# Kernel optimization log

Measured on AMD Instinct MI355X. Metric: run time of the kernel, lower is better.

The kernel has to match this reference:

```python
import jax, jax.numpy as jnp
import numpy as np

A_MIN = 0.001
EPS = 1e-08


def setup_inputs() -> dict:
    key = jax.random.key(0)
    k1, k2, k3, k4 = jax.random.split(key, 4)
    B, O, I = 512, 1024, 512
    x = jax.random.normal(k1, (B, I), dtype=jnp.float32)
    translation = jax.random.uniform(k2, (O, I), dtype=jnp.float32, minval=-1.0, maxval=1.0)
    scale_raw = jax.random.uniform(k3, (O, I), dtype=jnp.float32, minval=-2.0, maxval=0.0)
    weights = jax.random.normal(k4, (O, I), dtype=jnp.float32) * (1.0 / np.sqrt(I))
    return {"x": x, "translation": translation, "scale_raw": scale_raw, "weights": weights}


def reference(x, translation, scale_raw, weights):
    # x: (B, I); params: (O, I)
    scale = A_MIN + jax.nn.softplus(scale_raw)  # (O, I)
    # s: (B, O, I) broadcast intermediate
    s = (x[:, None, :] - translation[None, :, :]) / (scale[None, :, :] + EPS)
    s2 = s * s
    wavelet = (1.0 - s2) * jnp.exp(-0.5 * s2)  # mexican hat
    y = jnp.einsum('oi,boi->bo', weights, wavelet)  # reduce over in_features
    return y
```

## Files before the change

### kernel.cpp

```cpp
#include <hip/hip_runtime.h>


#define WL_A_MIN 0.001f
#define WL_EPS   1e-8f

constexpr int WL_B = 512;
constexpr int WL_O = 1024;
constexpr int WL_I = 512;

#define WL_SQK  0.84932180553704583800f
#define WL_IK   1.38629436111989061883f
#define WL_L2E  1.44269504088896340736f
#define WL_LN2  0.69314718055994530942f

typedef float v2f __attribute__((ext_vector_type(2)));

struct P3 { float nti, inv, w; };

__device__ __forceinline__ float fast_exp2(float a) {
#if __has_builtin(__builtin_amdgcn_exp2f)
    return __builtin_amdgcn_exp2f(a);
#else
    return exp2f(a);
#endif
}
__device__ __forceinline__ float fast_log2(float a) {
#if __has_builtin(__builtin_amdgcn_logf)
    return __builtin_amdgcn_logf(a);
#else
    return __log2f(a);
#endif
}
__device__ __forceinline__ float fast_rcp(float a) {
#if __has_builtin(__builtin_amdgcn_rcpf)
    return __builtin_amdgcn_rcpf(a);
#else
    return 1.0f / a;
#endif
}

__global__ __launch_bounds__(256) void wl_prep(
    const float* __restrict__ translation,
    const float* __restrict__ scale_raw,
    const float* __restrict__ weights,
    P3* __restrict__ pT3)
{
    __shared__ P3 lds[16 * 64];
    const int t  = threadIdx.x;
    const int o0 = blockIdx.x * 64;
    const int i0 = blockIdx.y * 16;

    {
        const int o_l = t >> 2;
        const int iq  = t & 3;
        const size_t g = (size_t)(o0 + o_l) * WL_I + (i0 + iq * 4);
        const float4 tv = *reinterpret_cast<const float4*>(translation + g);
        const float4 sv = *reinterpret_cast<const float4*>(scale_raw   + g);
        const float4 wv = *reinterpret_cast<const float4*>(weights     + g);
        const float tt[4] = {tv.x, tv.y, tv.z, tv.w};
        const float ss[4] = {sv.x, sv.y, sv.z, sv.w};
        const float ww[4] = {wv.x, wv.y, wv.z, wv.w};
        #pragma unroll
        for (int j = 0; j < 4; ++j) {
            float ex  = fast_exp2(ss[j] * WL_L2E);
            float sp  = fast_log2(1.0f + ex) * WL_LN2;
            float inv = fast_rcp(WL_A_MIN + sp + WL_EPS) * WL_SQK;
            P3 pv; pv.nti = -tt[j] * inv; pv.inv = inv; pv.w = ww[j];
            lds[(iq * 4 + j) * 64 + o_l] = pv;
        }
    }
    __syncthreads();
    {
        const int o_l = t & 63;
        const int r   = t >> 6;
        #pragma unroll
        for (int j = 0; j < 4; ++j) {
            const int i_l = r * 4 + j;
            pT3[(size_t)(i0 + i_l) * WL_O + (o0 + o_l)] = lds[i_l * 64 + o_l];
        }
    }
}

__global__ __launch_bounds__(512, 8) void wl_main(
    const float* __restrict__ x,
    const P3* __restrict__ pT3,
    float* __restrict__ out)
{
    __shared__ float smem[5120];

    const int tid  = threadIdx.x;
    const int lane = tid & 63;
    const int wid  = tid >> 6;
    const int o    = blockIdx.x * 64 + lane;
    const int b0   = blockIdx.y * 8;

    {
        const int b_l = tid & 7;
        const int seg = tid >> 3;
        const float* xg = &x[(size_t)(b0 + b_l) * WL_I + seg * 8];
        const float4 v0 = *reinterpret_cast<const float4*>(xg);
        const float4 v1 = *reinterpret_cast<const float4*>(xg + 4);
        const int base = seg * 64 + b_l;
        smem[base +  0] = v0.x;
        smem[base +  8] = v0.y;
        smem[base + 16] = v0.z;
        smem[base + 24] = v0.w;
        smem[base + 32] = v1.x;
        smem[base + 40] = v1.y;
        smem[base + 48] = v1.z;
        smem[base + 56] = v1.w;
    }
    __syncthreads();

    const P3*    pp = pT3 + (size_t)(wid * 64) * WL_O + o;
    const float* xr = &smem[wid * 64 * 8];

    v2f aE0 = {0.f,0.f}, aE1 = {0.f,0.f}, aE2 = {0.f,0.f}, aE3 = {0.f,0.f};
    v2f aU0 = {0.f,0.f}, aU1 = {0.f,0.f}, aU2 = {0.f,0.f}, aU3 = {0.f,0.f};

    #pragma unroll 4
    for (int ii = 0; ii < 64; ++ii) {
        const P3 p = *pp;  pp += WL_O;
        const float4 xa = *reinterpret_cast<const float4*>(xr);
        const float4 xb = *reinterpret_cast<const float4*>(xr + 4);
        xr += 8;

        v2f nti = {p.nti, p.nti};
        v2f inv = {p.inv, p.inv};
        v2f wv  = {p.w,  p.w};

        v2f x01 = {xa.x, xa.y};
        v2f x23 = {xa.z, xa.w};
        v2f x45 = {xb.x, xb.y};
        v2f x67 = {xb.z, xb.w};

        v2f s0 = __builtin_elementwise_fma(x01, inv, nti);
        v2f s1 = __builtin_elementwise_fma(x23, inv, nti);
        v2f s2 = __builtin_elementwise_fma(x45, inv, nti);
        v2f s3 = __builtin_elementwise_fma(x67, inv, nti);
        v2f u0 = s0 * s0;
        v2f u1 = s1 * s1;
        v2f u2 = s2 * s2;
        v2f u3 = s3 * s3;
        v2f e0 = {fast_exp2(-u0.x), fast_exp2(-u0.y)};
        v2f e1 = {fast_exp2(-u1.x), fast_exp2(-u1.y)};
        v2f e2 = {fast_exp2(-u2.x), fast_exp2(-u2.y)};
        v2f e3 = {fast_exp2(-u3.x), fast_exp2(-u3.y)};
        aE0 = __builtin_elementwise_fma(wv, e0, aE0);
        aE1 = __builtin_elementwise_fma(wv, e1, aE1);
        aE2 = __builtin_elementwise_fma(wv, e2, aE2);
        aE3 = __builtin_elementwise_fma(wv, e3, aE3);
        v2f ue0 = u0 * e0;
        v2f ue1 = u1 * e1;
        v2f ue2 = u2 * e2;
        v2f ue3 = u3 * e3;
        aU0 = __builtin_elementwise_fma(wv, ue0, aU0);
        aU1 = __builtin_elementwise_fma(wv, ue1, aU1);
        aU2 = __builtin_elementwise_fma(wv, ue2, aU2);
        aU3 = __builtin_elementwise_fma(wv, ue3, aU3);
    }

    __syncthreads();
    constexpr int RS = 20;
    if (wid >= 4) {
        float4* dst = reinterpret_cast<float4*>(&smem[((wid - 4) * 64 + lane) * RS]);
        dst[0] = make_float4(aE0.x, aE0.y, aE1.x, aE1.y);
        dst[1] = make_float4(aE2.x, aE2.y, aE3.x, aE3.y);
        dst[2] = make_float4(aU0.x, aU0.y, aU1.x, aU1.y);
        dst[3] = make_float4(aU2.x, aU2.y, aU3.x, aU3.y);
    }
    __syncthreads();
    if (wid < 4) {
        const float4* src = reinterpret_cast<const float4*>(&smem[(wid * 64 + lane) * RS]);
        const float4 v0 = src[0], v1 = src[1], v2 = src[2], v3 = src[3];
        aE0.x += v0.x; aE0.y += v0.y; aE1.x += v0.z; aE1.y += v0.w;
        aE2.x += v1.x; aE2.y += v1.y; aE3.x += v1.z; aE3.y += v1.w;
        aU0.x += v2.x; aU0.y += v2.y; aU1.x += v2.z; aU1.y += v2.w;
        aU2.x += v3.x; aU2.y += v3.y; aU3.x += v3.z; aU3.y += v3.w;
    }
    __syncthreads();
    if (wid >= 1 && wid < 4) {
        float4* dst = reinterpret_cast<float4*>(&smem[((wid - 1) * 64 + lane) * RS]);
        dst[0] = make_float4(aE0.x, aE0.y, aE1.x, aE1.y);
        dst[1] = make_float4(aE2.x, aE2.y, aE3.x, aE3.y);
        dst[2] = make_float4(aU0.x, aU0.y, aU1.x, aU1.y);
        dst[3] = make_float4(aU2.x, aU2.y, aU3.x, aU3.y);
    }
    __syncthreads();
    if (wid == 0) {
        float E[8] = {aE0.x, aE0.y, aE1.x, aE1.y, aE2.x, aE2.y, aE3.x, aE3.y};
        float U[8] = {aU0.x, aU0.y, aU1.x, aU1.y, aU2.x, aU2.y, aU3.x, aU3.y};
        #pragma unroll
        for (int q = 0; q < 3; ++q) {
            const float4* src = reinterpret_cast<const float4*>(&smem[(q * 64 + lane) * RS]);
            const float4 v0 = src[0], v1 = src[1], v2 = src[2], v3 = src[3];
            E[0] += v0.x; E[1] += v0.y; E[2] += v0.z; E[3] += v0.w;
            E[4] += v1.x; E[5] += v1.y; E[6] += v1.z; E[7] += v1.w;
            U[0] += v2.x; U[1] += v2.y; U[2] += v2.z; U[3] += v2.w;
            U[4] += v3.x; U[5] += v3.y; U[6] += v3.z; U[7] += v3.w;
        }
        #pragma unroll
        for (int k = 0; k < 8; ++k)
            out[(size_t)(b0 + k) * WL_O + o] = fmaf(-WL_IK, U[k], E[k]);
    }
}

extern "C" void kernel_launch(void* const* d_in, const int* in_sizes, int n_in,
                              void* d_out, int out_size, void* d_ws, size_t ws_size,
                              hipStream_t stream) {
    const float* x           = (const float*)d_in[0];
    const float* translation = (const float*)d_in[1];
    const float* scale_raw   = (const float*)d_in[2];
    const float* weights     = (const float*)d_in[3];
    float*       out         = (float*)d_out;
    P3*          pT3         = (P3*)d_ws;

    wl_prep<<<dim3(WL_O / 64, WL_I / 16), dim3(256), 0, stream>>>(
        translation, scale_raw, weights, pT3);

    wl_main<<<dim3(WL_O / 64, WL_B / 8), dim3(512), 0, stream>>>(
        x, pT3, out);
}
```

Baseline: 109.7 us.

## Split parameter layout into paired v2f arrays and use op_sel packed FMAs

The transposed parameter buffer changes from a 12-byte struct into an 8-byte (nti,inv) array plus a weight array that packs two input indices per element. Loads are aligned 8-byte vectors, and inline-asm v_pk_fma_f32 with op_sel broadcasts scalars inside the packed op. This is meant to remove the per-iteration v_mov broadcast instructions. The cross-wave reduction becomes a single padded LDS transpose with two barriers instead of a multi-stage tree. Launch bounds drop the waves-per-EU hint from 8 to 6, and shared memory grows, which may reduce occupancy.

```diff
diff --git a/kernel.cpp b/kernel.cpp
--- a/kernel.cpp
+++ b/kernel.cpp
@@ -39,11 +39,56 @@
 #endif
 }
 
+#define WL_STEP(PA, PW, OS, XA, XB)                                            \
+  do {                                                                         \
+    v2f x01 = {(XA).x, (XA).y}, x23 = {(XA).z, (XA).w};                        \
+    v2f x45 = {(XB).x, (XB).y}, x67 = {(XB).z, (XB).w};                        \
+    v2f s0_, s1_, s2_, s3_, u0_, u1_, u2_, u3_;                                \
+    v2f e0_, e1_, e2_, e3_, t0_, t1_, t2_, t3_;                                \
+    asm("v_pk_fma_f32 %0, %1, %2, %2 op_sel:[0,1,0] op_sel_hi:[1,1,0]"         \
+        : "=v"(s0_) : "v"(x01), "v"(PA));                                      \
+    asm("v_pk_fma_f32 %0, %1, %2, %2 op_sel:[0,1,0] op_sel_hi:[1,1,0]"         \
+        : "=v"(s1_) : "v"(x23), "v"(PA));                                      \
+    asm("v_pk_fma_f32 %0, %1, %2, %2 op_sel:[0,1,0] op_sel_hi:[1,1,0]"         \
+        : "=v"(s2_) : "v"(x45), "v"(PA));                                      \
+    asm("v_pk_fma_f32 %0, %1, %2, %2 op_sel:[0,1,0] op_sel_hi:[1,1,0]"         \
+        : "=v"(s3_) : "v"(x67), "v"(PA));                                      \
+    asm("v_pk_mul_f32 %0, %1, %1" : "=v"(u0_) : "v"(s0_));                     \
+    asm("v_pk_mul_f32 %0, %1, %1" : "=v"(u1_) : "v"(s1_));                     \
+    asm("v_pk_mul_f32 %0, %1, %1" : "=v"(u2_) : "v"(s2_));                     \
+    asm("v_pk_mul_f32 %0, %1, %1" : "=v"(u3_) : "v"(s3_));                     \
+    e0_.x = fast_exp2(-u0_.x); e0_.y = fast_exp2(-u0_.y);                      \
+    e1_.x = fast_exp2(-u1_.x); e1_.y = fast_exp2(-u1_.y);                      \
+    e2_.x = fast_exp2(-u2_.x); e2_.y = fast_exp2(-u2_.y);                      \
+    e3_.x = fast_exp2(-u3_.x); e3_.y = fast_exp2(-u3_.y);                      \
+    asm("v_pk_fma_f32 %0, %1, %2, %0 op_sel:[" OS ",0,0] op_sel_hi:[" OS ",1,1]" \
+        : "+v"(aE0) : "v"(PW), "v"(e0_));                                      \
+    asm("v_pk_fma_f32 %0, %1, %2, %0 op_sel:[" OS ",0,0] op_sel_hi:[" OS ",1,1]" \
+        : "+v"(aE1) : "v"(PW), "v"(e1_));                                      \
+    asm("v_pk_fma_f32 %0, %1, %2, %0 op_sel:[" OS ",0,0] op_sel_hi:[" OS ",1,1]" \
+        : "+v"(aE2) : "v"(PW), "v"(e2_));                                      \
+    asm("v_pk_fma_f32 %0, %1, %2, %0 op_sel:[" OS ",0,0] op_sel_hi:[" OS ",1,1]" \
+        : "+v"(aE3) : "v"(PW), "v"(e3_));                                      \
+    asm("v_pk_mul_f32 %0, %1, %2" : "=v"(t0_) : "v"(u0_), "v"(e0_));           \
+    asm("v_pk_mul_f32 %0, %1, %2" : "=v"(t1_) : "v"(u1_), "v"(e1_));           \
+    asm("v_pk_mul_f32 %0, %1, %2" : "=v"(t2_) : "v"(u2_), "v"(e2_));           \
+    asm("v_pk_mul_f32 %0, %1, %2" : "=v"(t3_) : "v"(u3_), "v"(e3_));           \
+    asm("v_pk_fma_f32 %0, %1, %2, %0 op_sel:[" OS ",0,0] op_sel_hi:[" OS ",1,1]" \
+        : "+v"(aU0) : "v"(PW), "v"(t0_));                                      \
+    asm("v_pk_fma_f32 %0, %1, %2, %0 op_sel:[" OS ",0,0] op_sel_hi:[" OS ",1,1]" \
+        : "+v"(aU1) : "v"(PW), "v"(t1_));                                      \
+    asm("v_pk_fma_f32 %0, %1, %2, %0 op_sel:[" OS ",0,0] op_sel_hi:[" OS ",1,1]" \
+        : "+v"(aU2) : "v"(PW), "v"(t2_));                                      \
+    asm("v_pk_fma_f32 %0, %1, %2, %0 op_sel:[" OS ",0,0] op_sel_hi:[" OS ",1,1]" \
+        : "+v"(aU3) : "v"(PW), "v"(t3_));                                      \
+  } while (0)
+
 __global__ __launch_bounds__(256) void wl_prep(
     const float* __restrict__ translation,
     const float* __restrict__ scale_raw,
     const float* __restrict__ weights,
-    P3* __restrict__ pT3)
+    v2f* __restrict__ A2,
+    v2f* __restrict__ W2)
 {
     __shared__ P3 lds[16 * 64];
     const int t  = threadIdx.x;
@@ -73,20 +118,26 @@
     {
         const int o_l = t & 63;
         const int r   = t >> 6;
-        #pragma unroll
-        for (int j = 0; j < 4; ++j) {
-            const int i_l = r * 4 + j;
-            pT3[(size_t)(i0 + i_l) * WL_O + (o0 + o_l)] = lds[i_l * 64 + o_l];
+        const int o   = o0 + o_l;
+        #pragma unroll
+        for (int jp = 0; jp < 2; ++jp) {
+            const int i_l = r * 4 + jp * 2;
+            P3 a = lds[i_l * 64 + o_l];
+            P3 b = lds[(i_l + 1) * 64 + o_l];
+            A2[(size_t)(i0 + i_l)     * WL_O + o] = (v2f){a.nti, a.inv};
+            A2[(size_t)(i0 + i_l + 1) * WL_O + o] = (v2f){b.nti, b.inv};
+            W2[(size_t)((i0 + i_l) >> 1) * WL_O + o] = (v2f){a.w, b.w};
         }
     }
 }
 
-__global__ __launch_bounds__(512, 8) void wl_main(
+__global__ __launch_bounds__(512, 6) void wl_main(
     const float* __restrict__ x,
-    const P3* __restrict__ pT3,
+    const v2f* __restrict__ A2,
+    const v2f* __restrict__ W2,
     float* __restrict__ out)
 {
-    __shared__ float smem[5120];
+    __shared__ float smem[16 * 513];
 
     const int tid  = threadIdx.x;
     const int lane = tid & 63;
@@ -112,96 +163,46 @@
     }
     __syncthreads();
 
-    const P3*    pp = pT3 + (size_t)(wid * 64) * WL_O + o;
+    const v2f* __restrict__ pA = A2 + (size_t)(wid * 64) * WL_O + o;
+    const v2f* __restrict__ pW = W2 + (size_t)(wid * 32) * WL_O + o;
     const float* xr = &smem[wid * 64 * 8];
 
     v2f aE0 = {0.f,0.f}, aE1 = {0.f,0.f}, aE2 = {0.f,0.f}, aE3 = {0.f,0.f};
     v2f aU0 = {0.f,0.f}, aU1 = {0.f,0.f}, aU2 = {0.f,0.f}, aU3 = {0.f,0.f};
 
-    #pragma unroll 4
-    for (int ii = 0; ii < 64; ++ii) {
-        const P3 p = *pp;  pp += WL_O;
-        const float4 xa = *reinterpret_cast<const float4*>(xr);
-        const float4 xb = *reinterpret_cast<const float4*>(xr + 4);
-        xr += 8;
-
-        v2f nti = {p.nti, p.nti};
-        v2f inv = {p.inv, p.inv};
-        v2f wv  = {p.w,  p.w};
-
-        v2f x01 = {xa.x, xa.y};
-        v2f x23 = {xa.z, xa.w};
-        v2f x45 = {xb.x, xb.y};
-        v2f x67 = {xb.z, xb.w};
-
-        v2f s0 = __builtin_elementwise_fma(x01, inv, nti);
-        v2f s1 = __builtin_elementwise_fma(x23, inv, nti);
-        v2f s2 = __builtin_elementwise_fma(x45, inv, nti);
-        v2f s3 = __builtin_elementwise_fma(x67, inv, nti);
-        v2f u0 = s0 * s0;
-        v2f u1 = s1 * s1;
-        v2f u2 = s2 * s2;
-        v2f u3 = s3 * s3;
-        v2f e0 = {fast_exp2(-u0.x), fast_exp2(-u0.y)};
-        v2f e1 = {fast_exp2(-u1.x), fast_exp2(-u1.y)};
-        v2f e2 = {fast_exp2(-u2.x), fast_exp2(-u2.y)};
-        v2f e3 = {fast_exp2(-u3.x), fast_exp2(-u3.y)};
-        aE0 = __builtin_elementwise_fma(wv, e0, aE0);
-        aE1 = __builtin_elementwise_fma(wv, e1, aE1);
-        aE2 = __builtin_elementwise_fma(wv, e2, aE2);
-        aE3 = __builtin_elementwise_fma(wv, e3, aE3);
-        v2f ue0 = u0 * e0;
-        v2f ue1 = u1 * e1;
-        v2f ue2 = u2 * e2;
-        v2f ue3 = u3 * e3;
-        aU0 = __builtin_elementwise_fma(wv, ue0, aU0);
-        aU1 = __builtin_elementwise_fma(wv, ue1, aU1);
-        aU2 = __builtin_elementwise_fma(wv, ue2, aU2);
-        aU3 = __builtin_elementwise_fma(wv, ue3, aU3);
-    }
-
-    __syncthreads();
-    constexpr int RS = 20;
-    if (wid >= 4) {
-        float4* dst = reinterpret_cast<float4*>(&smem[((wid - 4) * 64 + lane) * RS]);
-        dst[0] = make_float4(aE0.x, aE0.y, aE1.x, aE1.y);
-        dst[1] = make_float4(aE2.x, aE2.y, aE3.x, aE3.y);
-        dst[2] = make_float4(aU0.x, aU0.y, aU1.x, aU1.y);
-        dst[3] = make_float4(aU2.x, aU2.y, aU3.x, aU3.y);
-    }
-    __syncthreads();
-    if (wid < 4) {
-        const float4* src = reinterpret_cast<const float4*>(&smem[(wid * 64 + lane) * RS]);
-        const float4 v0 = src[0], v1 = src[1], v2 = src[2], v3 = src[3];
-        aE0.x += v0.x; aE0.y += v0.y; aE1.x += v0.z; aE1.y += v0.w;
-        aE2.x += v1.x; aE2.y += v1.y; aE3.x += v1.z; aE3.y += v1.w;
-        aU0.x += v2.x; aU0.y += v2.y; aU1.x += v2.z; aU1.y += v2.w;
-        aU2.x += v3.x; aU2.y += v3.y; aU3.x += v3.z; aU3.y += v3.w;
-    }
-    __syncthreads();
-    if (wid >= 1 && wid < 4) {
-        float4* dst = reinterpret_cast<float4*>(&smem[((wid - 1) * 64 + lane) * RS]);
-        dst[0] = make_float4(aE0.x, aE0.y, aE1.x, aE1.y);
-        dst[1] = make_float4(aE2.x, aE2.y, aE3.x, aE3.y);
-        dst[2] = make_float4(aU0.x, aU0.y, aU1.x, aU1.y);
-        dst[3] = make_float4(aU2.x, aU2.y, aU3.x, aU3.y);
-    }
-    __syncthreads();
-    if (wid == 0) {
-        float E[8] = {aE0.x, aE0.y, aE1.x, aE1.y, aE2.x, aE2.y, aE3.x, aE3.y};
-        float U[8] = {aU0.x, aU0.y, aU1.x, aU1.y, aU2.x, aU2.y, aU3.x, aU3.y};
-        #pragma unroll
-        for (int q = 0; q < 3; ++q) {
-            const float4* src = reinterpret_cast<const float4*>(&smem[(q * 64 + lane) * RS]);
-            const float4 v0 = src[0], v1 = src[1], v2 = src[2], v3 = src[3];
-            E[0] += v0.x; E[1] += v0.y; E[2] += v0.z; E[3] += v0.w;
-            E[4] += v1.x; E[5] += v1.y; E[6] += v1.z; E[7] += v1.w;
-            U[0] += v2.x; U[1] += v2.y; U[2] += v2.z; U[3] += v2.w;
-            U[4] += v3.x; U[5] += v3.y; U[6] += v3.z; U[7] += v3.w;
+    #pragma unroll 2
+    for (int g = 0; g < 32; ++g) {
+        const v2f pa0 = pA[0];
+        const v2f pa1 = pA[WL_O];
+        const v2f pw  = pW[0];
+        pA += 2 * WL_O;  pW += WL_O;
+        const float4 xa0 = ((const float4*)xr)[0];
+        const float4 xb0 = ((const float4*)xr)[1];
+        const float4 xa1 = ((const float4*)xr)[2];
+        const float4 xb1 = ((const float4*)xr)[3];
+        xr += 16;
+        WL_STEP(pa0, pw, "0", xa0, xb0);
+        WL_STEP(pa1, pw, "1", xa1, xb1);
+    }
+
+    __syncthreads();
+    {
+        const int c = wid * 64 + lane;
+        const float vals[16] = {aE0.x,aE0.y,aE1.x,aE1.y,aE2.x,aE2.y,aE3.x,aE3.y,
+                                aU0.x,aU0.y,aU1.x,aU1.y,aU2.x,aU2.y,aU3.x,aU3.y};
+        #pragma unroll
+        for (int k = 0; k < 16; ++k)
+            smem[k * 513 + c] = vals[k];
+    }
+    __syncthreads();
+    {
+        float E = 0.f, U = 0.f;
+        #pragma unroll
+        for (int sw = 0; sw < 8; ++sw) {
+            E += smem[wid * 513       + sw * 64 + lane];
+            U += smem[(8 + wid) * 513 + sw * 64 + lane];
         }
-        #pragma unroll
-        for (int k = 0; k < 8; ++k)
-            out[(size_t)(b0 + k) * WL_O + o] = fmaf(-WL_IK, U[k], E[k]);
+        out[(size_t)(b0 + wid) * WL_O + o] = fmaf(-WL_IK, U, E);
     }
 }
 
@@ -213,11 +214,12 @@
     const float* scale_raw   = (const float*)d_in[2];
     const float* weights     = (const float*)d_in[3];
     float*       out         = (float*)d_out;
-    P3*          pT3         = (P3*)d_ws;
+    v2f* A2 = (v2f*)d_ws;
+    v2f* W2 = (v2f*)((char*)d_ws + (size_t)WL_I * WL_O * sizeof(v2f));
 
     wl_prep<<<dim3(WL_O / 64, WL_I / 16), dim3(256), 0, stream>>>(
-        translation, scale_raw, weights, pT3);
+        translation, scale_raw, weights, A2, W2);
 
     wl_main<<<dim3(WL_O / 64, WL_B / 8), dim3(512), 0, stream>>>(
-        x, pT3, out);
-}
+        x, A2, W2, out);
+}
```

After: 110.2 us. Within noise of the previous version (+0.4%).
